# Performance work log

Hardware: AMD Instinct MI355X
Metric: run time of the kernel (lower is better)

The kernel has to match this reference:

```python
import jax, jax.numpy as jnp
import numpy as np

N, D = 4096, 128  # seq length / feature dim of x is N; head dim is D

def setup_inputs() -> dict:
    key = jax.random.key(0)
    k1, k2 = jax.random.split(key)
    x = jax.random.normal(k1, (N, N), dtype=jnp.float32)
    # nn.Linear(N, 3*d): weight [3d, N], bias [3d]; scale weight like torch init
    W = jax.random.normal(k2, (3 * D, N), dtype=jnp.float32) / jnp.sqrt(jnp.float32(N))
    b = jnp.zeros((3 * D,), dtype=jnp.float32)
    return {"x": x, "W": W, "b": b}

def reference(x, W, b):
    # QKV projection: [N, 3d]
    qkv = x @ W.T + b
    Q, K, V = jnp.split(qkv, 3, axis=-1)  # each [N, d]
    # The blockwise online-softmax double loop computes exactly
    # softmax(Q K^T) V with NO 1/sqrt(d) scaling (faithful to source).
    S = Q @ K.T                 # [N, N]
    P = jax.nn.softmax(S, axis=-1)
    return P @ V                # [N, d]
```

## Files before the change

### kernel.cpp

```cpp
#include <hip/hip_runtime.h>
#include <cstdint>
#include <cstddef>

typedef _Float16 f16;
typedef f16 f16x8 __attribute__((ext_vector_type(8)));
typedef f16 f16x4 __attribute__((ext_vector_type(4)));
typedef float f32x4 __attribute__((ext_vector_type(4)));

#define SEQ 4096
#define DH 128
#define QKV_LD 384
#define LOG2E 1.44269504f

__device__ __forceinline__ float fast_exp2(float x) {
#if __has_builtin(__builtin_amdgcn_exp2f)
  return __builtin_amdgcn_exp2f(x);
#else
  return exp2f(x);
#endif
}

__device__ __forceinline__ void gl_lds16(const void* g, void* l) {
  __builtin_amdgcn_global_load_lds((const __attribute__((address_space(1))) void*)g,
                                   (__attribute__((address_space(3))) void*)l, 16, 0, 0);
}

__global__ __launch_bounds__(256) void cvt_w_kernel(const float4* __restrict__ W,
                                                    f16x4* __restrict__ Wh) {
  int i = blockIdx.x * 256 + threadIdx.x;
  float4 v = W[i];
  f16x4 h; h[0] = (f16)v.x; h[1] = (f16)v.y; h[2] = (f16)v.z; h[3] = (f16)v.w;
  Wh[i] = h;
}

template <int SPLITS>
__global__ __launch_bounds__(256, 2) void gemm_qkv(const float* __restrict__ x,
                                                   const f16* __restrict__ Wh,
                                                   f16* __restrict__ part) {
  __shared__ __align__(16) f16 Ax[64][72];
  __shared__ __align__(16) f16 Bx[QKV_LD * 64];
  const int m0 = blockIdx.x * 64;
  const int split = blockIdx.y;
  const int kc = SEQ / SPLITS;
  const int k0 = split * kc;
  const int tid = threadIdx.x;
  const int lane = tid & 63;
  const int wave = tid >> 6;
  const int nb = wave * 96;
  const int l15 = lane & 15, quad = lane >> 4;

  f32x4 acc[4][6] = {};

  for (int kt = k0; kt < k0 + kc; kt += 64) {
#pragma unroll
    for (int r = 0; r < 12; ++r) {
      int c = r * 256 + tid;
      int row = c >> 3, ch = c & 7;
      const f16* src = &Wh[(size_t)row * SEQ + kt + ((ch ^ (row & 7)) << 3)];
      gl_lds16(src, &Bx[(size_t)c << 3]);
    }
#pragma unroll
    for (int r = 0; r < 4; ++r) {
      int c = r * 256 + tid;
      int row = c >> 4, col = (c & 15) * 4;
      float4 v = *(const float4*)&x[(size_t)(m0 + row) * SEQ + kt + col];
      f16x4 h; h[0] = (f16)v.x; h[1] = (f16)v.y; h[2] = (f16)v.z; h[3] = (f16)v.w;
      *(f16x4*)&Ax[row][col] = h;
    }
    __syncthreads();
#pragma unroll
    for (int ks = 0; ks < 2; ++ks) {
      f16x8 a[4], bb[6];
#pragma unroll
      for (int t = 0; t < 4; ++t)
        a[t] = *(const f16x8*)&Ax[t * 16 + l15][ks * 32 + quad * 8];
#pragma unroll
      for (int t = 0; t < 6; ++t) {
        int n = nb + t * 16 + l15;
        int ch = (ks * 4 + quad) ^ (l15 & 7);
        bb[t] = *(const f16x8*)&Bx[((size_t)n << 6) + (ch << 3)];
      }
#pragma unroll
      for (int mt = 0; mt < 4; ++mt)
#pragma unroll
        for (int nt = 0; nt < 6; ++nt)
          acc[mt][nt] = __builtin_amdgcn_mfma_f32_16x16x32_f16(a[mt], bb[nt], acc[mt][nt], 0, 0, 0);
    }
    __syncthreads();
  }

  f16* pw = part + (size_t)split * SEQ * QKV_LD;
#pragma unroll
  for (int mt = 0; mt < 4; ++mt) {
#pragma unroll
    for (int nt = 0; nt < 6; ++nt) {
      int col = nb + nt * 16 + l15;
      int rowbase = m0 + mt * 16 + quad * 4;
#pragma unroll
      for (int rr = 0; rr < 4; ++rr)
        pw[(size_t)(rowbase + rr) * QKV_LD + col] = (f16)acc[mt][nt][rr];
    }
  }
}

template <int SPLITS>
__global__ __launch_bounds__(256) void reduce_qkv(const f16* __restrict__ part,
                                                  const float* __restrict__ bias,
                                                  f16* __restrict__ qkv) {
  int i = (blockIdx.x * 256 + threadIdx.x) * 8;
  float acc[8] = {};
#pragma unroll
  for (int s = 0; s < SPLITS; ++s) {
    f16x8 p = *(const f16x8*)&part[(size_t)s * SEQ * QKV_LD + i];
#pragma unroll
    for (int j = 0; j < 8; ++j) acc[j] += (float)p[j];
  }
  int col = i % QKV_LD;
  f16x8 o;
#pragma unroll
  for (int j = 0; j < 8; ++j) o[j] = (f16)(acc[j] + bias[col + j]);
  *(f16x8*)&qkv[i] = o;
}

__global__ __launch_bounds__(256) void transpose_v(const f16* __restrict__ qkv,
                                                   f16* __restrict__ Vt) {
  __shared__ __align__(16) f16 T[64][72];
  const int r0 = blockIdx.x * 64;
  const int c0 = blockIdx.y * 64;
  const int tid = threadIdx.x;
#pragma unroll
  for (int rep = 0; rep < 2; ++rep) {
    int idx = rep * 256 + tid;
    int row = idx >> 3, col = (idx & 7) * 8;
    *(f16x8*)&T[row][col] = *(const f16x8*)&qkv[(size_t)(r0 + row) * QKV_LD + 256 + c0 + col];
  }
  __syncthreads();
#pragma unroll
  for (int rep = 0; rep < 2; ++rep) {
    int idx = rep * 256 + tid;
    int cc = idx >> 3, rb = (idx & 7) * 8;
    f16x8 o;
#pragma unroll
    for (int j = 0; j < 8; ++j) o[j] = T[rb + j][cc];
    *(f16x8*)&Vt[(size_t)(c0 + cc) * SEQ + r0 + rb] = o;
  }
}

#define NSPLIT 16
#define KVRANGE (SEQ / NSPLIT)

__global__ __launch_bounds__(256, 2) void attn_partial(const f16* __restrict__ qkv,
                                                       const f16* __restrict__ Vt,
                                                       f16* __restrict__ Op,
                                                       float* __restrict__ ml) {
  __shared__ __align__(16) f16 Ks[64][136];
  __shared__ __align__(16) f16 Vs[128][72];
  __shared__ __align__(16) f16 Ps[4][32][72];

  const int q0 = blockIdx.x * 128;
  const int split = blockIdx.y;
  const int kv0 = split * KVRANGE;
  const int tid = threadIdx.x;
  const int lane = tid & 63, wave = tid >> 6;
  const int l15 = lane & 15, quad = lane >> 4;
  const int mbase = q0 + wave * 32;

  f16x8 qf[2][4];
#pragma unroll
  for (int mt = 0; mt < 2; ++mt)
#pragma unroll
    for (int ks = 0; ks < 4; ++ks) {
      f16x8 q = *(const f16x8*)&qkv[(size_t)(mbase + mt * 16 + l15) * QKV_LD + ks * 32 + quad * 8];
      qf[mt][ks] = q * (f16)LOG2E;
    }

  f32x4 oacc[2][8] = {};
  float mrow[2] = {-1e30f, -1e30f};
  float lrow[2] = {0.f, 0.f};

  for (int it = 0; it < KVRANGE / 64; ++it) {
    const int k0 = kv0 + it * 64;
#pragma unroll
    for (int r = 0; r < 4; ++r) {
      int c = tid + r * 256;
      int row = c >> 4, col = (c & 15) * 8;
      *(f16x8*)&Ks[row][col] = *(const f16x8*)&qkv[(size_t)(k0 + row) * QKV_LD + DH + col];
    }
#pragma unroll
    for (int r = 0; r < 4; ++r) {
      int c = tid + r * 256;
      int row = c >> 3, col = (c & 7) * 8;
      *(f16x8*)&Vs[row][col] = *(const f16x8*)&Vt[(size_t)row * SEQ + k0 + col];
    }
    __syncthreads();

    f32x4 st[4][2] = {};
#pragma unroll
    for (int ks = 0; ks < 4; ++ks) {
      f16x8 kf[4];
#pragma unroll
      for (int kt = 0; kt < 4; ++kt)
        kf[kt] = *(const f16x8*)&Ks[kt * 16 + l15][ks * 32 + quad * 8];
#pragma unroll
      for (int kt = 0; kt < 4; ++kt)
#pragma unroll
        for (int mt = 0; mt < 2; ++mt)
          st[kt][mt] = __builtin_amdgcn_mfma_f32_16x16x32_f16(kf[kt], qf[mt][ks], st[kt][mt], 0, 0, 0);
    }

    float al[2];
#pragma unroll
    for (int mt = 0; mt < 2; ++mt) {
      float v = -1e30f;
#pragma unroll
      for (int kt = 0; kt < 4; ++kt)
#pragma unroll
        for (int rr = 0; rr < 4; ++rr) v = fmaxf(v, st[kt][mt][rr]);
      v = fmaxf(v, __shfl_xor(v, 16));
      v = fmaxf(v, __shfl_xor(v, 32));
      float mnew = fmaxf(mrow[mt], v);
      al[mt] = fast_exp2(mrow[mt] - mnew);
      mrow[mt] = mnew;
      float ls = 0.f;
#pragma unroll
      for (int kt = 0; kt < 4; ++kt) {
        f16x4 pk;
#pragma unroll
        for (int rr = 0; rr < 4; ++rr) {
          float p = fast_exp2(st[kt][mt][rr] - mnew);
          ls += p;
          pk[rr] = (f16)p;
        }
        *(f16x4*)&Ps[wave][mt * 16 + l15][kt * 16 + quad * 4] = pk;
      }
      ls += __shfl_xor(ls, 16);
      ls += __shfl_xor(ls, 32);
      lrow[mt] = lrow[mt] * al[mt] + ls;
    }

    float alr[2][4];
#pragma unroll
    for (int mt = 0; mt < 2; ++mt)
#pragma unroll
      for (int rr = 0; rr < 4; ++rr)
        alr[mt][rr] = __shfl(al[mt], quad * 4 + rr);
#pragma unroll
    for (int mt = 0; mt < 2; ++mt)
#pragma unroll
      for (int dt = 0; dt < 8; ++dt)
#pragma unroll
        for (int rr = 0; rr < 4; ++rr)
          oacc[mt][dt][rr] *= alr[mt][rr];

#pragma unroll
    for (int kk = 0; kk < 2; ++kk) {
      f16x8 pf[2];
#pragma unroll
      for (int mt = 0; mt < 2; ++mt)
        pf[mt] = *(const f16x8*)&Ps[wave][mt * 16 + l15][kk * 32 + quad * 8];
#pragma unroll
      for (int dt = 0; dt < 8; ++dt) {
        f16x8 vf = *(const f16x8*)&Vs[dt * 16 + l15][kk * 32 + quad * 8];
#pragma unroll
        for (int mt = 0; mt < 2; ++mt)
          oacc[mt][dt] = __builtin_amdgcn_mfma_f32_16x16x32_f16(pf[mt], vf, oacc[mt][dt], 0, 0, 0);
      }
    }
    __syncthreads();
  }

#pragma unroll
  for (int mt = 0; mt < 2; ++mt)
#pragma unroll
    for (int dt = 0; dt < 8; ++dt)
#pragma unroll
      for (int rr = 0; rr < 4; ++rr) {
        int row = mbase + mt * 16 + quad * 4 + rr;
        Op[((size_t)split * SEQ + row) * DH + dt * 16 + l15] = (f16)oacc[mt][dt][rr];
      }
  if (quad == 0) {
#pragma unroll
    for (int mt = 0; mt < 2; ++mt) {
      int row = mbase + mt * 16 + l15;
      ml[((size_t)split * SEQ + row) * 2 + 0] = mrow[mt];
      ml[((size_t)split * SEQ + row) * 2 + 1] = lrow[mt];
    }
  }
}

__global__ __launch_bounds__(256) void combine_kernel(const f16* __restrict__ Op,
                                                      const float* __restrict__ ml,
                                                      float* __restrict__ out) {
  int idx = blockIdx.x * 256 + threadIdx.x;
  int row = idx >> 7;
  float ms[NSPLIT], ls[NSPLIT];
  float M = -1e30f;
#pragma unroll
  for (int s = 0; s < NSPLIT; ++s) {
    ms[s] = ml[((size_t)s * SEQ + row) * 2 + 0];
    ls[s] = ml[((size_t)s * SEQ + row) * 2 + 1];
    M = fmaxf(M, ms[s]);
  }
  float L = 0.f, o = 0.f;
#pragma unroll
  for (int s = 0; s < NSPLIT; ++s) {
    float w = fast_exp2(ms[s] - M);
    L += ls[s] * w;
    o += w * (float)Op[(size_t)s * SEQ * DH + idx];
  }
  out[idx] = o / L;
}

extern "C" void kernel_launch(void* const* d_in, const int* in_sizes, int n_in,
                              void* d_out, int out_size, void* d_ws, size_t ws_size,
                              hipStream_t stream) {
  const float* x = (const float*)d_in[0];
  const float* W = (const float*)d_in[1];
  const float* b = (const float*)d_in[2];
  float* out = (float*)d_out;
  char* ws = (char*)d_ws;

  f16*   Wh   = (f16*)(ws);
  f16*   qkv  = (f16*)(ws + (3u << 20));
  f16*   Vt   = (f16*)(ws + (6u << 20));
  float* ml   = (float*)(ws + (7u << 20));
  char*  scr  = ws + (7u << 20) + (1u << 19);
  f16*   part = (f16*)scr;
  f16*   Op   = (f16*)scr;

  cvt_w_kernel<<<(384 * 4096 / 4) / 256, 256, 0, stream>>>((const float4*)W, (f16x4*)Wh);

  bool big = ws_size >= ((size_t)31u << 20) + ((size_t)1u << 19);
  if (big) {
    gemm_qkv<8><<<dim3(SEQ / 64, 8), 256, 0, stream>>>(x, Wh, part);
    reduce_qkv<8><<<SEQ * QKV_LD / 8 / 256, 256, 0, stream>>>(part, b, qkv);
  } else {
    gemm_qkv<4><<<dim3(SEQ / 64, 4), 256, 0, stream>>>(x, Wh, part);
    reduce_qkv<4><<<SEQ * QKV_LD / 8 / 256, 256, 0, stream>>>(part, b, qkv);
  }
  transpose_v<<<dim3(SEQ / 64, DH / 64), 256, 0, stream>>>(qkv, Vt);
  attn_partial<<<dim3(SEQ / 128, NSPLIT), 256, 0, stream>>>(qkv, Vt, Op, ml);
  combine_kernel<<<(SEQ * DH) / 256, 256, 0, stream>>>(Op, ml, out);
}
```

Measured before the change: 152.0 us.

## Read GEMM weights directly from global, shrink attention tiles, async-swizzle K/V loads

The QKV GEMM stops staging W tiles in LDS and has each wave read its B fragments straight from global memory, with launch bounds raised to 3 blocks per CU. Its split-K count grows to 16 when the workspace is large enough. The attention kernel now takes 64 queries per block (16 per wave) instead of 128, which cuts registers and LDS and raises occupancy. K and V tiles are loaded with async global-to-LDS copies into XOR-swizzled layouts. The cost is lost reuse of W across waves, uncoalesced global fragment reads, more partial-sum traffic, and K/V tiles loaded twice as often per query.

```diff
diff --git a/kernel.cpp b/kernel.cpp
--- a/kernel.cpp
+++ b/kernel.cpp
@@ -34,11 +34,10 @@
 }
 
 template <int SPLITS>
-__global__ __launch_bounds__(256, 2) void gemm_qkv(const float* __restrict__ x,
+__global__ __launch_bounds__(256, 3) void gemm_qkv(const float* __restrict__ x,
                                                    const f16* __restrict__ Wh,
                                                    f16* __restrict__ part) {
   __shared__ __align__(16) f16 Ax[64][72];
-  __shared__ __align__(16) f16 Bx[QKV_LD * 64];
   const int m0 = blockIdx.x * 64;
   const int split = blockIdx.y;
   const int kc = SEQ / SPLITS;
@@ -53,13 +52,6 @@
 
   for (int kt = k0; kt < k0 + kc; kt += 64) {
 #pragma unroll
-    for (int r = 0; r < 12; ++r) {
-      int c = r * 256 + tid;
-      int row = c >> 3, ch = c & 7;
-      const f16* src = &Wh[(size_t)row * SEQ + kt + ((ch ^ (row & 7)) << 3)];
-      gl_lds16(src, &Bx[(size_t)c << 3]);
-    }
-#pragma unroll
     for (int r = 0; r < 4; ++r) {
       int c = r * 256 + tid;
       int row = c >> 4, col = (c & 15) * 4;
@@ -75,11 +67,8 @@
       for (int t = 0; t < 4; ++t)
         a[t] = *(const f16x8*)&Ax[t * 16 + l15][ks * 32 + quad * 8];
 #pragma unroll
-      for (int t = 0; t < 6; ++t) {
-        int n = nb + t * 16 + l15;
-        int ch = (ks * 4 + quad) ^ (l15 & 7);
-        bb[t] = *(const f16x8*)&Bx[((size_t)n << 6) + (ch << 3)];
-      }
+      for (int t = 0; t < 6; ++t)
+        bb[t] = *(const f16x8*)&Wh[(size_t)(nb + t * 16 + l15) * SEQ + kt + ks * 32 + quad * 8];
 #pragma unroll
       for (int mt = 0; mt < 4; ++mt)
 #pragma unroll
@@ -149,142 +138,124 @@
 #define NSPLIT 16
 #define KVRANGE (SEQ / NSPLIT)
 
-__global__ __launch_bounds__(256, 2) void attn_partial(const f16* __restrict__ qkv,
+__global__ __launch_bounds__(256, 3) void attn_partial(const f16* __restrict__ qkv,
                                                        const f16* __restrict__ Vt,
                                                        f16* __restrict__ Op,
                                                        float* __restrict__ ml) {
-  __shared__ __align__(16) f16 Ks[64][136];
-  __shared__ __align__(16) f16 Vs[128][72];
-  __shared__ __align__(16) f16 Ps[4][32][72];
-
-  const int q0 = blockIdx.x * 128;
+  __shared__ __align__(16) f16 Ks[64 * 128];
+  __shared__ __align__(16) f16 Vs[128 * 64];
+  __shared__ __align__(16) f16 Ps[4][16][72];
+
+  const int q0 = blockIdx.x * 64;
   const int split = blockIdx.y;
   const int kv0 = split * KVRANGE;
   const int tid = threadIdx.x;
   const int lane = tid & 63, wave = tid >> 6;
   const int l15 = lane & 15, quad = lane >> 4;
-  const int mbase = q0 + wave * 32;
-
-  f16x8 qf[2][4];
-#pragma unroll
-  for (int mt = 0; mt < 2; ++mt)
-#pragma unroll
-    for (int ks = 0; ks < 4; ++ks) {
-      f16x8 q = *(const f16x8*)&qkv[(size_t)(mbase + mt * 16 + l15) * QKV_LD + ks * 32 + quad * 8];
-      qf[mt][ks] = q * (f16)LOG2E;
-    }
-
-  f32x4 oacc[2][8] = {};
-  float mrow[2] = {-1e30f, -1e30f};
-  float lrow[2] = {0.f, 0.f};
+  const int mbase = q0 + wave * 16;
+
+  f16x8 qf[4];
+#pragma unroll
+  for (int ks = 0; ks < 4; ++ks) {
+    f16x8 q = *(const f16x8*)&qkv[(size_t)(mbase + l15) * QKV_LD + ks * 32 + quad * 8];
+    qf[ks] = q * (f16)LOG2E;
+  }
+
+  f32x4 oacc[8] = {};
+  float mrow = -1e30f, lrow = 0.f;
 
   for (int it = 0; it < KVRANGE / 64; ++it) {
     const int k0 = kv0 + it * 64;
 #pragma unroll
     for (int r = 0; r < 4; ++r) {
-      int c = tid + r * 256;
-      int row = c >> 4, col = (c & 15) * 8;
-      *(f16x8*)&Ks[row][col] = *(const f16x8*)&qkv[(size_t)(k0 + row) * QKV_LD + DH + col];
+      int c = r * 256 + tid;
+      int row = c >> 4, ch = c & 15;
+      gl_lds16(&qkv[(size_t)(k0 + row) * QKV_LD + DH + ((ch ^ (row & 7)) << 3)],
+               &Ks[(size_t)c << 3]);
     }
 #pragma unroll
     for (int r = 0; r < 4; ++r) {
-      int c = tid + r * 256;
-      int row = c >> 3, col = (c & 7) * 8;
-      *(f16x8*)&Vs[row][col] = *(const f16x8*)&Vt[(size_t)row * SEQ + k0 + col];
+      int c = r * 256 + tid;
+      int row = c >> 3, ch = c & 7;
+      gl_lds16(&Vt[(size_t)row * SEQ + k0 + ((ch ^ (row & 7)) << 3)],
+               &Vs[(size_t)c << 3]);
     }
     __syncthreads();
 
-    f32x4 st[4][2] = {};
+    f32x4 st[4] = {};
 #pragma unroll
     for (int ks = 0; ks < 4; ++ks) {
       f16x8 kf[4];
 #pragma unroll
+      for (int kt = 0; kt < 4; ++kt) {
+        int row = kt * 16 + l15;
+        int ch = (ks * 4 + quad) ^ (row & 7);
+        kf[kt] = *(const f16x8*)&Ks[row * 128 + ch * 8];
+      }
+#pragma unroll
       for (int kt = 0; kt < 4; ++kt)
-        kf[kt] = *(const f16x8*)&Ks[kt * 16 + l15][ks * 32 + quad * 8];
-#pragma unroll
-      for (int kt = 0; kt < 4; ++kt)
-#pragma unroll
-        for (int mt = 0; mt < 2; ++mt)
-          st[kt][mt] = __builtin_amdgcn_mfma_f32_16x16x32_f16(kf[kt], qf[mt][ks], st[kt][mt], 0, 0, 0);
-    }
-
-    float al[2];
-#pragma unroll
-    for (int mt = 0; mt < 2; ++mt) {
-      float v = -1e30f;
-#pragma unroll
-      for (int kt = 0; kt < 4; ++kt)
-#pragma unroll
-        for (int rr = 0; rr < 4; ++rr) v = fmaxf(v, st[kt][mt][rr]);
-      v = fmaxf(v, __shfl_xor(v, 16));
-      v = fmaxf(v, __shfl_xor(v, 32));
-      float mnew = fmaxf(mrow[mt], v);
-      al[mt] = fast_exp2(mrow[mt] - mnew);
-      mrow[mt] = mnew;
-      float ls = 0.f;
-#pragma unroll
-      for (int kt = 0; kt < 4; ++kt) {
-        f16x4 pk;
-#pragma unroll
-        for (int rr = 0; rr < 4; ++rr) {
-          float p = fast_exp2(st[kt][mt][rr] - mnew);
-          ls += p;
-          pk[rr] = (f16)p;
-        }
-        *(f16x4*)&Ps[wave][mt * 16 + l15][kt * 16 + quad * 4] = pk;
+        st[kt] = __builtin_amdgcn_mfma_f32_16x16x32_f16(kf[kt], qf[ks], st[kt], 0, 0, 0);
+    }
+
+    float v = -1e30f;
+#pragma unroll
+    for (int kt = 0; kt < 4; ++kt)
+#pragma unroll
+      for (int rr = 0; rr < 4; ++rr) v = fmaxf(v, st[kt][rr]);
+    v = fmaxf(v, __shfl_xor(v, 16));
+    v = fmaxf(v, __shfl_xor(v, 32));
+    float mnew = fmaxf(mrow, v);
+    float al = fast_exp2(mrow - mnew);
+    mrow = mnew;
+    float ls = 0.f;
+#pragma unroll
+    for (int kt = 0; kt < 4; ++kt) {
+      f16x4 pk;
+#pragma unroll
+      for (int rr = 0; rr < 4; ++rr) {
+        float p = fast_exp2(st[kt][rr] - mnew);
+        ls += p;
+        pk[rr] = (f16)p;
       }
-      ls += __shfl_xor(ls, 16);
-      ls += __shfl_xor(ls, 32);
-      lrow[mt] = lrow[mt] * al[mt] + ls;
-    }
-
-    float alr[2][4];
-#pragma unroll
-    for (int mt = 0; mt < 2; ++mt)
-#pragma unroll
-      for (int rr = 0; rr < 4; ++rr)
-        alr[mt][rr] = __shfl(al[mt], quad * 4 + rr);
-#pragma unroll
-    for (int mt = 0; mt < 2; ++mt)
-#pragma unroll
-      for (int dt = 0; dt < 8; ++dt)
-#pragma unroll
-        for (int rr = 0; rr < 4; ++rr)
-          oacc[mt][dt][rr] *= alr[mt][rr];
+      *(f16x4*)&Ps[wave][l15][kt * 16 + quad * 4] = pk;
+    }
+    ls += __shfl_xor(ls, 16);
+    ls += __shfl_xor(ls, 32);
+    lrow = lrow * al + ls;
+
+    float alr[4];
+#pragma unroll
+    for (int rr = 0; rr < 4; ++rr) alr[rr] = __shfl(al, quad * 4 + rr);
+#pragma unroll
+    for (int dt = 0; dt < 8; ++dt)
+#pragma unroll
+      for (int rr = 0; rr < 4; ++rr) oacc[dt][rr] *= alr[rr];
 
 #pragma unroll
     for (int kk = 0; kk < 2; ++kk) {
-      f16x8 pf[2];
-#pragma unroll
-      for (int mt = 0; mt < 2; ++mt)
-        pf[mt] = *(const f16x8*)&Ps[wave][mt * 16 + l15][kk * 32 + quad * 8];
+      f16x8 pf = *(const f16x8*)&Ps[wave][l15][kk * 32 + quad * 8];
 #pragma unroll
       for (int dt = 0; dt < 8; ++dt) {
-        f16x8 vf = *(const f16x8*)&Vs[dt * 16 + l15][kk * 32 + quad * 8];
-#pragma unroll
-        for (int mt = 0; mt < 2; ++mt)
-          oacc[mt][dt] = __builtin_amdgcn_mfma_f32_16x16x32_f16(pf[mt], vf, oacc[mt][dt], 0, 0, 0);
+        int row = dt * 16 + l15;
+        int ch = (kk * 4 + quad) ^ (row & 7);
+        f16x8 vf = *(const f16x8*)&Vs[row * 64 + ch * 8];
+        oacc[dt] = __builtin_amdgcn_mfma_f32_16x16x32_f16(pf, vf, oacc[dt], 0, 0, 0);
       }
     }
     __syncthreads();
   }
 
 #pragma unroll
-  for (int mt = 0; mt < 2; ++mt)
-#pragma unroll
-    for (int dt = 0; dt < 8; ++dt)
-#pragma unroll
-      for (int rr = 0; rr < 4; ++rr) {
-        int row = mbase + mt * 16 + quad * 4 + rr;
-        Op[((size_t)split * SEQ + row) * DH + dt * 16 + l15] = (f16)oacc[mt][dt][rr];
-      }
+  for (int dt = 0; dt < 8; ++dt)
+#pragma unroll
+    for (int rr = 0; rr < 4; ++rr) {
+      int row = mbase + quad * 4 + rr;
+      Op[((size_t)split * SEQ + row) * DH + dt * 16 + l15] = (f16)oacc[dt][rr];
+    }
   if (quad == 0) {
-#pragma unroll
-    for (int mt = 0; mt < 2; ++mt) {
-      int row = mbase + mt * 16 + l15;
-      ml[((size_t)split * SEQ + row) * 2 + 0] = mrow[mt];
-      ml[((size_t)split * SEQ + row) * 2 + 1] = lrow[mt];
-    }
+    int row = mbase + l15;
+    ml[((size_t)split * SEQ + row) * 2 + 0] = mrow;
+    ml[((size_t)split * SEQ + row) * 2 + 1] = lrow;
   }
 }
 
@@ -330,15 +301,15 @@
 
   cvt_w_kernel<<<(384 * 4096 / 4) / 256, 256, 0, stream>>>((const float4*)W, (f16x4*)Wh);
 
-  bool big = ws_size >= ((size_t)31u << 20) + ((size_t)1u << 19);
+  bool big = ws_size >= ((size_t)56u << 20);
   if (big) {
+    gemm_qkv<16><<<dim3(SEQ / 64, 16), 256, 0, stream>>>(x, Wh, part);
+    reduce_qkv<16><<<SEQ * QKV_LD / 8 / 256, 256, 0, stream>>>(part, b, qkv);
+  } else {
     gemm_qkv<8><<<dim3(SEQ / 64, 8), 256, 0, stream>>>(x, Wh, part);
     reduce_qkv<8><<<SEQ * QKV_LD / 8 / 256, 256, 0, stream>>>(part, b, qkv);
-  } else {
-    gemm_qkv<4><<<dim3(SEQ / 64, 4), 256, 0, stream>>>(x, Wh, part);
-    reduce_qkv<4><<<SEQ * QKV_LD / 8 / 256, 256, 0, stream>>>(part, b, qkv);
   }
   transpose_v<<<dim3(SEQ / 64, DH / 64), 256, 0, stream>>>(qkv, Vt);
-  attn_partial<<<dim3(SEQ / 128, NSPLIT), 256, 0, stream>>>(qkv, Vt, Op, ml);
+  attn_partial<<<dim3(SEQ / 64, NSPLIT), 256, 0, stream>>>(qkv, Vt, Op, ml);
   combine_kernel<<<(SEQ * DH) / 256, 256, 0, stream>>>(Op, ml, out);
 }
```

Measured after the change: 212.2 us. 39.6% more time.
